# Kernel tuning notes

Hardware: AMD Instinct MI355X
Metric: run time of the kernel (lower is better)

Reference implementation:

```python
import jax, jax.numpy as jnp
import numpy as np

B, T, N_IN, N_REC, N_OUT = 64, 1000, 128, 1024, 64
PROP_E = 0.8
DT_OVER_TAU = 1.0 / 10.0  # dt=1, Tau=10


def dale_mask(n):
    e = int(PROP_E * n)
    m = np.tile(np.array([1.0] * e + [-1.0] * (n - e), dtype=np.float32), (n, 1))
    np.fill_diagonal(m, 0.0)
    return jnp.asarray(m)


def setup_inputs() -> dict:
    key = jax.random.key(0)
    ks = jax.random.split(key, 6)
    s = 1.0 / np.sqrt(N_REC)
    return {
        "x": jax.random.normal(ks[0], (B, T, N_IN), jnp.float32),
        "Wahx": jax.random.normal(ks[1], (N_REC, N_IN), jnp.float32) / np.sqrt(N_IN),
        "Wahh": jax.random.normal(ks[2], (N_REC, N_REC), jnp.float32) * s,
        "Wyh": jax.random.normal(ks[3], (N_OUT, N_REC), jnp.float32) * s,
        "bah": jax.random.normal(ks[4], (N_REC,), jnp.float32) * 0.01,
        "by": jax.random.normal(ks[5], (N_OUT,), jnp.float32) * 0.01,
        "ah0": jnp.zeros((N_REC,), jnp.float32),
        "mask": dale_mask(N_REC),
    }


def retanh(a):
    # 'retanh' activation: max(tanh(a), 0)
    return jnp.maximum(jnp.tanh(a), 0.0)


def reference(x, Wahx, Wahh, Wyh, bah, by, ah0, mask):
    # Dale-constrained effective recurrent weight: abs(W) * sign-mask
    Weff = jnp.abs(Wahh) * mask                       # [N, N]
    # precompute input drive for all timesteps: [B, T, N]
    xin = jnp.einsum('bti,ni->btn', x, Wahx) + bah
    ah_init = jnp.broadcast_to(ah0, (B, N_REC))

    def step(ah, xt):
        h = retanh(ah)
        ah_new = ah + DT_OVER_TAU * (-ah + h @ Weff.T + xt)
        return ah_new, retanh(ah_new)

    _, hs = jax.lax.scan(step, ah_init, jnp.swapaxes(xin, 0, 1))  # hs: [T, B, N]
    y = jnp.einsum('tbn,on->bto', hs, Wyh) + by       # [B, T, n_output]
    return y
```

## Files before the change

kernel.cpp:

```cpp
#include <hip/hip_runtime.h>
#include <hip/hip_bf16.h>
#include <stdint.h>


#define B_    64
#define T_    1000
#define NIN   128
#define NREC  1024
#define NOUT  64
#define GROUPS  4
#define MEMBERS 64
#define BPG   16
#define NSL   16

#define DT    0.1f

typedef short  bf16x8 __attribute__((ext_vector_type(8)));
typedef float  f32x4  __attribute__((ext_vector_type(4)));

#define SCOPE __HIP_MEMORY_SCOPE_AGENT

#define XB_OFF     0
#define XB_BYTES   (B_ * T_ * NIN * 2)
#define HBUF_OFF   (XB_OFF + XB_BYTES)
#define HBUF_BYTES (GROUPS * 2 * BPG * NREC * 2)

#define TAGMASK 0x8000000080000000ull

union U16B { unsigned long long q[2]; bf16x8 s; };

__device__ __forceinline__ unsigned short f2bf(float f) {
    unsigned u = __float_as_uint(f);
    unsigned r = u + 0x7fffu + ((u >> 16) & 1u);
    return (unsigned short)(r >> 16);
}
__device__ __forceinline__ unsigned pack2(float lo, float hi) {
    return (unsigned)f2bf(lo) | ((unsigned)f2bf(hi) << 16);
}

__global__ void cast_x_kernel(const float* __restrict__ x, unsigned short* __restrict__ xb, int n4) {
    int i = blockIdx.x * blockDim.x + threadIdx.x;
    int stride = gridDim.x * blockDim.x;
    for (; i < n4; i += stride) {
        float4 v = ((const float4*)x)[i];
        unsigned lo = pack2(v.x, v.y);
        unsigned hi = pack2(v.z, v.w);
        ((uint2*)xb)[i] = make_uint2(lo, hi);
    }
}

__global__ __launch_bounds__(256, 1)
void rnn_main(const float* __restrict__ Wahx, const float* __restrict__ Wahh,
              const float* __restrict__ Wyh,  const float* __restrict__ bah,
              const float* __restrict__ by,   const float* __restrict__ ah0,
              const float* __restrict__ mask,
              const unsigned short* __restrict__ xb,
              unsigned short* __restrict__ hbuf,
              float* __restrict__ y)
{
    __shared__ unsigned short weff[NSL * NREC];
    __shared__ unsigned short wahxs[NSL * NIN];
    __shared__ unsigned short wyhs[NREC];
    __shared__ float red[4][2][64][4];

    const int tid  = threadIdx.x;
    const int w    = tid >> 6;
    const int lane = tid & 63;
    const int bid  = blockIdx.x;
    const int g    = bid & 3;
    const int m    = bid >> 2;

    for (int cc = 0; cc < 8; ++cc) {
        int cid = cc * 256 + tid;
        int rl = cid >> 7;
        int k  = (cid & 127) * 8;
        const float* wr = Wahh + (m * NSL + rl) * NREC + k;
        const float* mr = mask + (m * NSL + rl) * NREC + k;
        float4 a0 = *(const float4*)wr;     float4 a1 = *(const float4*)(wr + 4);
        float4 m0 = *(const float4*)mr;     float4 m1 = *(const float4*)(mr + 4);
        uint4 pk;
        pk.x = pack2(fabsf(a0.x) * m0.x, fabsf(a0.y) * m0.y);
        pk.y = pack2(fabsf(a0.z) * m0.z, fabsf(a0.w) * m0.w);
        pk.z = pack2(fabsf(a1.x) * m1.x, fabsf(a1.y) * m1.y);
        pk.w = pack2(fabsf(a1.z) * m1.z, fabsf(a1.w) * m1.w);
        int byte = (rl * 2048 + k * 2) ^ ((rl & 7) << 4);
        *(uint4*)((char*)weff + byte) = pk;
    }
    {
        int rl = tid >> 4;
        int k  = (tid & 15) * 8;
        const float* wr = Wahx + (m * NSL + rl) * NIN + k;
        float4 a0 = *(const float4*)wr;  float4 a1 = *(const float4*)(wr + 4);
        uint4 pk;
        pk.x = pack2(a0.x, a0.y); pk.y = pack2(a0.z, a0.w);
        pk.z = pack2(a1.x, a1.y); pk.w = pack2(a1.z, a1.w);
        int byte = (rl * 256 + k * 2) ^ ((rl & 7) << 4);
        *(uint4*)((char*)wahxs + byte) = pk;
    }
    if (tid < 128) {
        int k = tid * 8;
        const float* wr = Wyh + m * NREC + k;
        float4 a0 = *(const float4*)wr;  float4 a1 = *(const float4*)(wr + 4);
        uint4 pk;
        pk.x = pack2(a0.x, a0.y); pk.y = pack2(a0.z, a0.w);
        pk.z = pack2(a1.x, a1.y); pk.w = pack2(a1.z, a1.w);
        *(uint4*)((char*)wyhs + k * 2) = pk;
    }

    const int b_loc = tid >> 4;
    const int nl    = tid & 15;
    const int n_g   = m * NSL + nl;
    float ahv  = ah0[n_g];
    float bahv = bah[n_g];
    float byv  = by[m];

    {
        float th = tanhf(ahv);
        float h0 = th > 0.f ? th : 0.f;
        unsigned hb = f2bf(h0);
        unsigned nb = __shfl_down(hb, 1);
        if ((nl & 1) == 0) {
            unsigned w32 = hb | (nb << 16);
            int eidx = ((g * 2 + 0) * BPG + b_loc) * NREC + n_g;
            __hip_atomic_store((unsigned*)hbuf + (eidx >> 1), w32, __ATOMIC_RELAXED, SCOPE);
        }
    }
    __syncthreads();

    const int bcol = lane & 15;
    const int khi  = (lane >> 4) * 8;

    for (int t = 0; t <= T_; ++t) {
        bf16x8 xf, axf;
        if (t < T_) {
            int i = w * 32 + khi;
            xf = *(const bf16x8*)(xb + ((size_t)(g * BPG + bcol) * T_ + t) * NIN + i);
            int byte = (bcol * 256 + i * 2) ^ ((bcol & 7) << 4);
            axf = *(const bf16x8*)((const char*)wahxs + byte);
        }

        const int slot = t & 1;
        const unsigned long long want = ((t >> 1) & 1) ? TAGMASK : 0ull;
        const unsigned long long* hq =
            (const unsigned long long*)(hbuf + ((g * 2 + slot) * BPG + bcol) * NREC);

        U16B u[8];
        unsigned pend = 0xFFu;
        for (;;) {
            #pragma unroll
            for (int c = 0; c < 8; ++c) {
                if (pend & (1u << c)) {
                    int k = w * 256 + c * 32 + khi;
                    u[c].q[0] = __hip_atomic_load(hq + (k >> 2),     __ATOMIC_RELAXED, SCOPE);
                    u[c].q[1] = __hip_atomic_load(hq + (k >> 2) + 1, __ATOMIC_RELAXED, SCOPE);
                }
            }
            unsigned np = 0u;
            #pragma unroll
            for (int c = 0; c < 8; ++c) {
                if (pend & (1u << c)) {
                    unsigned long long d = ((u[c].q[0] ^ want) | (u[c].q[1] ^ want)) & TAGMASK;
                    np |= d ? (1u << c) : 0u;
                }
            }
            pend = np;
            if (!__any(pend != 0u)) break;
            __builtin_amdgcn_s_sleep(1);
        }
        bf16x8 bfrag[8];
        #pragma unroll
        for (int c = 0; c < 8; ++c) {
            u[c].q[0] &= ~TAGMASK;
            u[c].q[1] &= ~TAGMASK;
            bfrag[c] = u[c].s;
        }

        f32x4 acc = {0.f, 0.f, 0.f, 0.f};
        if (t < T_) {
            f32x4 a0 = {0.f, 0.f, 0.f, 0.f};
            f32x4 a1 = {0.f, 0.f, 0.f, 0.f};
            a0 = __builtin_amdgcn_mfma_f32_16x16x32_bf16(axf, xf, a0, 0, 0, 0);
            #pragma unroll
            for (int c = 0; c < 4; ++c) {
                int k = w * 256 + c * 32 + khi;
                int byte = (bcol * 2048 + k * 2) ^ ((bcol & 7) << 4);
                bf16x8 af = *(const bf16x8*)((const char*)weff + byte);
                a0 = __builtin_amdgcn_mfma_f32_16x16x32_bf16(af, bfrag[c], a0, 0, 0, 0);
            }
            #pragma unroll
            for (int c = 4; c < 8; ++c) {
                int k = w * 256 + c * 32 + khi;
                int byte = (bcol * 2048 + k * 2) ^ ((bcol & 7) << 4);
                bf16x8 af = *(const bf16x8*)((const char*)weff + byte);
                a1 = __builtin_amdgcn_mfma_f32_16x16x32_bf16(af, bfrag[c], a1, 0, 0, 0);
            }
            acc = a0 + a1;
        }

        *(f32x4*)&red[w][0][lane][0] = acc;
        __syncthreads();

        if (t < T_) {
            int src = ((nl >> 2) << 4) | b_loc;
            int reg = nl & 3;
            float r = red[0][0][src][reg] + red[1][0][src][reg]
                    + red[2][0][src][reg] + red[3][0][src][reg];
            ahv = 0.9f * ahv + DT * (r + bahv);
            float th = tanhf(ahv);
            float h  = th > 0.f ? th : 0.f;
            unsigned hb = f2bf(h);
            unsigned nb = __shfl_down(hb, 1);
            if ((nl & 1) == 0) {
                unsigned tagw = (unsigned)(((t + 1) >> 1) & 1) << 31;
                unsigned w32 = hb | (nb << 16) | tagw;
                int eidx = ((g * 2 + (slot ^ 1)) * BPG + b_loc) * NREC + n_g;
                __hip_atomic_store((unsigned*)hbuf + (eidx >> 1), w32, __ATOMIC_RELAXED, SCOPE);
            }
        }

        if (t >= 1) {
            f32x4 accy = {0.f, 0.f, 0.f, 0.f};
            #pragma unroll
            for (int c = 0; c < 8; ++c) {
                int k = w * 256 + c * 32 + khi;
                bf16x8 af = *(const bf16x8*)((const char*)wyhs + k * 2);
                accy = __builtin_amdgcn_mfma_f32_16x16x32_bf16(af, bfrag[c], accy, 0, 0, 0);
            }
            *(f32x4*)&red[w][1][lane][0] = accy;
            __syncthreads();
            if (tid < BPG) {
                float yv = red[0][1][tid][0] + red[1][1][tid][0]
                         + red[2][1][tid][0] + red[3][1][tid][0] + byv;
                __builtin_nontemporal_store(yv, &y[((size_t)(g * BPG + tid) * T_ + (t - 1)) * NOUT + m]);
            }
        } else {
            __syncthreads();
        }
    }
}

extern "C" void kernel_launch(void* const* d_in, const int* in_sizes, int n_in,
                              void* d_out, int out_size, void* d_ws, size_t ws_size,
                              hipStream_t stream) {
    const float* x    = (const float*)d_in[0];
    const float* Wahx = (const float*)d_in[1];
    const float* Wahh = (const float*)d_in[2];
    const float* Wyh  = (const float*)d_in[3];
    const float* bah  = (const float*)d_in[4];
    const float* by   = (const float*)d_in[5];
    const float* ah0  = (const float*)d_in[6];
    const float* mask = (const float*)d_in[7];
    float* y = (float*)d_out;
    char* ws = (char*)d_ws;
    unsigned short* xb   = (unsigned short*)(ws + XB_OFF);
    unsigned short* hbuf = (unsigned short*)(ws + HBUF_OFF);

    (void)in_sizes; (void)n_in; (void)out_size; (void)ws_size;

    hipMemsetAsync(hbuf, 0xFF, HBUF_BYTES, stream);
    cast_x_kernel<<<dim3(2048), dim3(256), 0, stream>>>(x, xb, (B_ * T_ * NIN) / 4);
    rnn_main<<<dim3(GROUPS * MEMBERS), dim3(256), 0, stream>>>(
        Wahx, Wahh, Wyh, bah, by, ah0, mask, xb, hbuf, y);
}
```

Baseline: 3.175 ms.

## Halve workgroup count by assigning 32 recurrent neurons per workgroup

Each workgroup now owns 32 recurrent neurons and two output channels instead of 16 and one, so only 128 workgroups take part in the per-step cross-workgroup handoff through global memory instead of 256. Every wave issues twice the MFMAs per step on the same loaded h fragments, and each thread updates two neuron states. The aim is to cut synchronization and polling traffic and to reuse each h load across more work. The cost is a longer per-step critical path inside each workgroup and more LDS use for weights.

```diff
diff --git a/kernel.cpp b/kernel.cpp
--- a/kernel.cpp
+++ b/kernel.cpp
@@ -9,9 +9,9 @@
 #define NREC  1024
 #define NOUT  64
 #define GROUPS  4
-#define MEMBERS 64
+#define MEMBERS 32
 #define BPG   16
-#define NSL   16
+#define NSL   32
 
 #define DT    0.1f
 
@@ -60,8 +60,8 @@
 {
     __shared__ unsigned short weff[NSL * NREC];
     __shared__ unsigned short wahxs[NSL * NIN];
-    __shared__ unsigned short wyhs[NREC];
-    __shared__ float red[4][2][64][4];
+    __shared__ unsigned short wyhs[2 * NREC];
+    __shared__ float red[4][3][64][4];
 
     const int tid  = threadIdx.x;
     const int w    = tid >> 6;
@@ -70,7 +70,7 @@
     const int g    = bid & 3;
     const int m    = bid >> 2;
 
-    for (int cc = 0; cc < 8; ++cc) {
+    for (int cc = 0; cc < 16; ++cc) {
         int cid = cc * 256 + tid;
         int rl = cid >> 7;
         int k  = (cid & 127) * 8;
@@ -86,9 +86,10 @@
         int byte = (rl * 2048 + k * 2) ^ ((rl & 7) << 4);
         *(uint4*)((char*)weff + byte) = pk;
     }
-    {
-        int rl = tid >> 4;
-        int k  = (tid & 15) * 8;
+    for (int cc = 0; cc < 2; ++cc) {
+        int cid = cc * 256 + tid;
+        int rl = cid >> 4;
+        int k  = (cid & 15) * 8;
         const float* wr = Wahx + (m * NSL + rl) * NIN + k;
         float4 a0 = *(const float4*)wr;  float4 a1 = *(const float4*)(wr + 4);
         uint4 pk;
@@ -97,32 +98,35 @@
         int byte = (rl * 256 + k * 2) ^ ((rl & 7) << 4);
         *(uint4*)((char*)wahxs + byte) = pk;
     }
-    if (tid < 128) {
-        int k = tid * 8;
-        const float* wr = Wyh + m * NREC + k;
+    {
+        int row = tid >> 7;
+        int k   = (tid & 127) * 8;
+        const float* wr = Wyh + (2 * m + row) * NREC + k;
         float4 a0 = *(const float4*)wr;  float4 a1 = *(const float4*)(wr + 4);
         uint4 pk;
         pk.x = pack2(a0.x, a0.y); pk.y = pack2(a0.z, a0.w);
         pk.z = pack2(a1.x, a1.y); pk.w = pack2(a1.z, a1.w);
-        *(uint4*)((char*)wyhs + k * 2) = pk;
+        *(uint4*)((char*)wyhs + (row * 1024 + k) * 2) = pk;
     }
 
     const int b_loc = tid >> 4;
     const int nl    = tid & 15;
-    const int n_g   = m * NSL + nl;
-    float ahv  = ah0[n_g];
-    float bahv = bah[n_g];
-    float byv  = by[m];
+    const int n_g0  = m * NSL + nl;
+    const int n_g1  = n_g0 + 16;
+    float ahv0 = ah0[n_g0], ahv1 = ah0[n_g1];
+    float bahv0 = bah[n_g0], bahv1 = bah[n_g1];
+    float byv0 = by[2 * m], byv1 = by[2 * m + 1];
 
     {
-        float th = tanhf(ahv);
-        float h0 = th > 0.f ? th : 0.f;
-        unsigned hb = f2bf(h0);
-        unsigned nb = __shfl_down(hb, 1);
+        float t0 = tanhf(ahv0);  float h0 = t0 > 0.f ? t0 : 0.f;
+        float t1 = tanhf(ahv1);  float h1 = t1 > 0.f ? t1 : 0.f;
+        unsigned hb0 = f2bf(h0), hb1 = f2bf(h1);
+        unsigned nb0 = __shfl_down(hb0, 1), nb1 = __shfl_down(hb1, 1);
         if ((nl & 1) == 0) {
-            unsigned w32 = hb | (nb << 16);
-            int eidx = ((g * 2 + 0) * BPG + b_loc) * NREC + n_g;
-            __hip_atomic_store((unsigned*)hbuf + (eidx >> 1), w32, __ATOMIC_RELAXED, SCOPE);
+            int e0 = ((g * 2 + 0) * BPG + b_loc) * NREC + n_g0;
+            int e1 = ((g * 2 + 0) * BPG + b_loc) * NREC + n_g1;
+            __hip_atomic_store((unsigned*)hbuf + (e0 >> 1), hb0 | (nb0 << 16), __ATOMIC_RELAXED, SCOPE);
+            __hip_atomic_store((unsigned*)hbuf + (e1 >> 1), hb1 | (nb1 << 16), __ATOMIC_RELAXED, SCOPE);
         }
     }
     __syncthreads();
@@ -131,12 +135,14 @@
     const int khi  = (lane >> 4) * 8;
 
     for (int t = 0; t <= T_; ++t) {
-        bf16x8 xf, axf;
+        bf16x8 xf, axf0, axf1;
         if (t < T_) {
             int i = w * 32 + khi;
             xf = *(const bf16x8*)(xb + ((size_t)(g * BPG + bcol) * T_ + t) * NIN + i);
-            int byte = (bcol * 256 + i * 2) ^ ((bcol & 7) << 4);
-            axf = *(const bf16x8*)((const char*)wahxs + byte);
+            int by0 = (bcol * 256 + i * 2) ^ ((bcol & 7) << 4);
+            int by1 = ((bcol + 16) * 256 + i * 2) ^ ((bcol & 7) << 4);
+            axf0 = *(const bf16x8*)((const char*)wahxs + by0);
+            axf1 = *(const bf16x8*)((const char*)wahxs + by1);
         }
 
         const int slot = t & 1;
@@ -175,46 +181,62 @@
             bfrag[c] = u[c].s;
         }
 
-        f32x4 acc = {0.f, 0.f, 0.f, 0.f};
+        f32x4 acc0 = {0.f, 0.f, 0.f, 0.f};
+        f32x4 acc1 = {0.f, 0.f, 0.f, 0.f};
         if (t < T_) {
-            f32x4 a0 = {0.f, 0.f, 0.f, 0.f};
-            f32x4 a1 = {0.f, 0.f, 0.f, 0.f};
-            a0 = __builtin_amdgcn_mfma_f32_16x16x32_bf16(axf, xf, a0, 0, 0, 0);
+            f32x4 p00 = {0.f, 0.f, 0.f, 0.f}, p01 = {0.f, 0.f, 0.f, 0.f};
+            f32x4 p10 = {0.f, 0.f, 0.f, 0.f}, p11 = {0.f, 0.f, 0.f, 0.f};
+            p00 = __builtin_amdgcn_mfma_f32_16x16x32_bf16(axf0, xf, p00, 0, 0, 0);
+            p10 = __builtin_amdgcn_mfma_f32_16x16x32_bf16(axf1, xf, p10, 0, 0, 0);
             #pragma unroll
             for (int c = 0; c < 4; ++c) {
                 int k = w * 256 + c * 32 + khi;
-                int byte = (bcol * 2048 + k * 2) ^ ((bcol & 7) << 4);
-                bf16x8 af = *(const bf16x8*)((const char*)weff + byte);
-                a0 = __builtin_amdgcn_mfma_f32_16x16x32_bf16(af, bfrag[c], a0, 0, 0, 0);
+                int by0 = (bcol * 2048 + k * 2) ^ ((bcol & 7) << 4);
+                int by1 = ((bcol + 16) * 2048 + k * 2) ^ ((bcol & 7) << 4);
+                bf16x8 af0 = *(const bf16x8*)((const char*)weff + by0);
+                bf16x8 af1 = *(const bf16x8*)((const char*)weff + by1);
+                p00 = __builtin_amdgcn_mfma_f32_16x16x32_bf16(af0, bfrag[c], p00, 0, 0, 0);
+                p10 = __builtin_amdgcn_mfma_f32_16x16x32_bf16(af1, bfrag[c], p10, 0, 0, 0);
             }
             #pragma unroll
             for (int c = 4; c < 8; ++c) {
                 int k = w * 256 + c * 32 + khi;
-                int byte = (bcol * 2048 + k * 2) ^ ((bcol & 7) << 4);
-                bf16x8 af = *(const bf16x8*)((const char*)weff + byte);
-                a1 = __builtin_amdgcn_mfma_f32_16x16x32_bf16(af, bfrag[c], a1, 0, 0, 0);
-            }
-            acc = a0 + a1;
-        }
-
-        *(f32x4*)&red[w][0][lane][0] = acc;
+                int by0 = (bcol * 2048 + k * 2) ^ ((bcol & 7) << 4);
+                int by1 = ((bcol + 16) * 2048 + k * 2) ^ ((bcol & 7) << 4);
+                bf16x8 af0 = *(const bf16x8*)((const char*)weff + by0);
+                bf16x8 af1 = *(const bf16x8*)((const char*)weff + by1);
+                p01 = __builtin_amdgcn_mfma_f32_16x16x32_bf16(af0, bfrag[c], p01, 0, 0, 0);
+                p11 = __builtin_amdgcn_mfma_f32_16x16x32_bf16(af1, bfrag[c], p11, 0, 0, 0);
+            }
+            acc0 = p00 + p01;
+            acc1 = p10 + p11;
+        }
+
+        *(f32x4*)&red[w][0][lane][0] = acc0;
+        *(f32x4*)&red[w][1][lane][0] = acc1;
         __syncthreads();
 
         if (t < T_) {
             int src = ((nl >> 2) << 4) | b_loc;
             int reg = nl & 3;
-            float r = red[0][0][src][reg] + red[1][0][src][reg]
-                    + red[2][0][src][reg] + red[3][0][src][reg];
-            ahv = 0.9f * ahv + DT * (r + bahv);
-            float th = tanhf(ahv);
-            float h  = th > 0.f ? th : 0.f;
-            unsigned hb = f2bf(h);
-            unsigned nb = __shfl_down(hb, 1);
+            float r0 = red[0][0][src][reg] + red[1][0][src][reg]
+                     + red[2][0][src][reg] + red[3][0][src][reg];
+            float r1 = red[0][1][src][reg] + red[1][1][src][reg]
+                     + red[2][1][src][reg] + red[3][1][src][reg];
+            ahv0 = 0.9f * ahv0 + DT * (r0 + bahv0);
+            ahv1 = 0.9f * ahv1 + DT * (r1 + bahv1);
+            float t0 = tanhf(ahv0);  float h0 = t0 > 0.f ? t0 : 0.f;
+            float t1 = tanhf(ahv1);  float h1 = t1 > 0.f ? t1 : 0.f;
+            unsigned hb0 = f2bf(h0), hb1 = f2bf(h1);
+            unsigned nb0 = __shfl_down(hb0, 1), nb1 = __shfl_down(hb1, 1);
             if ((nl & 1) == 0) {
                 unsigned tagw = (unsigned)(((t + 1) >> 1) & 1) << 31;
-                unsigned w32 = hb | (nb << 16) | tagw;
-                int eidx = ((g * 2 + (slot ^ 1)) * BPG + b_loc) * NREC + n_g;
-                __hip_atomic_store((unsigned*)hbuf + (eidx >> 1), w32, __ATOMIC_RELAXED, SCOPE);
+                int e0 = ((g * 2 + (slot ^ 1)) * BPG + b_loc) * NREC + n_g0;
+                int e1 = ((g * 2 + (slot ^ 1)) * BPG + b_loc) * NREC + n_g1;
+                __hip_atomic_store((unsigned*)hbuf + (e0 >> 1),
+                                   hb0 | (nb0 << 16) | tagw, __ATOMIC_RELAXED, SCOPE);
+                __hip_atomic_store((unsigned*)hbuf + (e1 >> 1),
+                                   hb1 | (nb1 << 16) | tagw, __ATOMIC_RELAXED, SCOPE);
             }
         }
 
@@ -223,15 +245,22 @@
             #pragma unroll
             for (int c = 0; c < 8; ++c) {
                 int k = w * 256 + c * 32 + khi;
-                bf16x8 af = *(const bf16x8*)((const char*)wyhs + k * 2);
-                accy = __builtin_amdgcn_mfma_f32_16x16x32_bf16(af, bfrag[c], accy, 0, 0, 0);
-            }
-            *(f32x4*)&red[w][1][lane][0] = accy;
+                bf16x8 yaf = {0, 0, 0, 0, 0, 0, 0, 0};
+                if (bcol < 2)
+                    yaf = *(const bf16x8*)((const char*)wyhs + (bcol * 1024 + k) * 2);
+                accy = __builtin_amdgcn_mfma_f32_16x16x32_bf16(yaf, bfrag[c], accy, 0, 0, 0);
+            }
+            *(f32x4*)&red[w][2][lane][0] = accy;
             __syncthreads();
             if (tid < BPG) {
-                float yv = red[0][1][tid][0] + red[1][1][tid][0]
-                         + red[2][1][tid][0] + red[3][1][tid][0] + byv;
-                __builtin_nontemporal_store(yv, &y[((size_t)(g * BPG + tid) * T_ + (t - 1)) * NOUT + m]);
+                float yv0 = red[0][2][tid][0] + red[1][2][tid][0]
+                          + red[2][2][tid][0] + red[3][2][tid][0] + byv0;
+                float yv1 = red[0][2][tid][1] + red[1][2][tid][1]
+                          + red[2][2][tid][1] + red[3][2][tid][1] + byv1;
+                union { float f[2]; double d; } uu;
+                uu.f[0] = yv0; uu.f[1] = yv1;
+                __builtin_nontemporal_store(uu.d,
+                    (double*)&y[((size_t)(g * BPG + tid) * T_ + (t - 1)) * NOUT + 2 * m]);
             }
         } else {
             __syncthreads();
```

Result: slower. 3.543 ms (+11.6%).

## Give each wave a full batch slice and the full K, removing LDS reduction barriers

Applied to the files above, without the earlier changes.

The grid shrinks from 256 blocks (4 batch groups × 64 neuron slices) to 64 blocks. Each wave now owns 16 batch rows and accumulates over the full 1024-wide recurrent K in registers. This removes the cross-wave LDS reduction and both __syncthreads per timestep, and writes h as 64-bit tagged stores straight from the MFMA output layout. The cost is 4x more MFMA and polling-load work per wave, higher register pressure (32 bf16x8 fragments), and only a quarter as many CUs in use.

```diff
diff --git a/kernel.cpp b/kernel.cpp
--- a/kernel.cpp
+++ b/kernel.cpp
@@ -8,9 +8,7 @@
 #define NIN   128
 #define NREC  1024
 #define NOUT  64
-#define GROUPS  4
 #define MEMBERS 64
-#define BPG   16
 #define NSL   16
 
 #define DT    0.1f
@@ -23,7 +21,7 @@
 #define XB_OFF     0
 #define XB_BYTES   (B_ * T_ * NIN * 2)
 #define HBUF_OFF   (XB_OFF + XB_BYTES)
-#define HBUF_BYTES (GROUPS * 2 * BPG * NREC * 2)
+#define HBUF_BYTES (2 * B_ * NREC * 2)
 
 #define TAGMASK 0x8000000080000000ull
 
@@ -61,14 +59,11 @@
     __shared__ unsigned short weff[NSL * NREC];
     __shared__ unsigned short wahxs[NSL * NIN];
     __shared__ unsigned short wyhs[NREC];
-    __shared__ float red[4][2][64][4];
 
     const int tid  = threadIdx.x;
     const int w    = tid >> 6;
     const int lane = tid & 63;
-    const int bid  = blockIdx.x;
-    const int g    = bid & 3;
-    const int m    = bid >> 2;
+    const int m    = blockIdx.x;
 
     for (int cc = 0; cc < 8; ++cc) {
         int cid = cc * 256 + tid;
@@ -107,134 +102,118 @@
         *(uint4*)((char*)wyhs + k * 2) = pk;
     }
 
-    const int b_loc = tid >> 4;
-    const int nl    = tid & 15;
-    const int n_g   = m * NSL + nl;
-    float ahv  = ah0[n_g];
-    float bahv = bah[n_g];
-    float byv  = by[m];
-
-    {
-        float th = tanhf(ahv);
-        float h0 = th > 0.f ? th : 0.f;
-        unsigned hb = f2bf(h0);
-        unsigned nb = __shfl_down(hb, 1);
-        if ((nl & 1) == 0) {
-            unsigned w32 = hb | (nb << 16);
-            int eidx = ((g * 2 + 0) * BPG + b_loc) * NREC + n_g;
-            __hip_atomic_store((unsigned*)hbuf + (eidx >> 1), w32, __ATOMIC_RELAXED, SCOPE);
-        }
-    }
-    __syncthreads();
-
     const int bcol = lane & 15;
     const int khi  = (lane >> 4) * 8;
+    const int bg   = w * 16 + bcol;
+    const int nr0  = m * NSL + (lane >> 4) * 4;
+
+    f32x4 ahv, bahv;
+    #pragma unroll
+    for (int r = 0; r < 4; ++r) { ahv[r] = ah0[nr0 + r]; bahv[r] = bah[nr0 + r]; }
+    const float byv = by[m];
+
+    unsigned long long* const hq_base = (unsigned long long*)hbuf;
+
+    {
+        float h[4];
+        #pragma unroll
+        for (int r = 0; r < 4; ++r) { float th = tanhf(ahv[r]); h[r] = th > 0.f ? th : 0.f; }
+        unsigned lo = (unsigned)f2bf(h[0]) | ((unsigned)f2bf(h[1]) << 16);
+        unsigned hi = (unsigned)f2bf(h[2]) | ((unsigned)f2bf(h[3]) << 16);
+        unsigned long long wq = (unsigned long long)lo | ((unsigned long long)hi << 32);
+        __hip_atomic_store(hq_base + (((size_t)bg) << 8) + (nr0 >> 2), wq,
+                           __ATOMIC_RELAXED, SCOPE);
+    }
+    __syncthreads();
 
     for (int t = 0; t <= T_; ++t) {
-        bf16x8 xf, axf;
+        bf16x8 xf[4];
         if (t < T_) {
-            int i = w * 32 + khi;
-            xf = *(const bf16x8*)(xb + ((size_t)(g * BPG + bcol) * T_ + t) * NIN + i);
-            int byte = (bcol * 256 + i * 2) ^ ((bcol & 7) << 4);
-            axf = *(const bf16x8*)((const char*)wahxs + byte);
+            const unsigned short* xp = xb + ((size_t)bg * T_ + t) * NIN;
+            #pragma unroll
+            for (int cx = 0; cx < 4; ++cx)
+                xf[cx] = *(const bf16x8*)(xp + cx * 32 + khi);
         }
 
         const int slot = t & 1;
         const unsigned long long want = ((t >> 1) & 1) ? TAGMASK : 0ull;
-        const unsigned long long* hq =
-            (const unsigned long long*)(hbuf + ((g * 2 + slot) * BPG + bcol) * NREC);
-
-        U16B u[8];
-        unsigned pend = 0xFFu;
+        const unsigned long long* bq =
+            hq_base + (((size_t)(slot * B_ + bg)) << 8) + (khi >> 2);
+
+        U16B u[32];
+        unsigned pend = 0xFFFFFFFFu;
         for (;;) {
             #pragma unroll
-            for (int c = 0; c < 8; ++c) {
-                if (pend & (1u << c)) {
-                    int k = w * 256 + c * 32 + khi;
-                    u[c].q[0] = __hip_atomic_load(hq + (k >> 2),     __ATOMIC_RELAXED, SCOPE);
-                    u[c].q[1] = __hip_atomic_load(hq + (k >> 2) + 1, __ATOMIC_RELAXED, SCOPE);
-                }
+            for (int c = 0; c < 32; ++c) if (pend & (1u << c)) {
+                u[c].q[0] = __hip_atomic_load(bq + c * 8,     __ATOMIC_RELAXED, SCOPE);
+                u[c].q[1] = __hip_atomic_load(bq + c * 8 + 1, __ATOMIC_RELAXED, SCOPE);
             }
             unsigned np = 0u;
             #pragma unroll
-            for (int c = 0; c < 8; ++c) {
-                if (pend & (1u << c)) {
-                    unsigned long long d = ((u[c].q[0] ^ want) | (u[c].q[1] ^ want)) & TAGMASK;
-                    np |= d ? (1u << c) : 0u;
-                }
+            for (int c = 0; c < 32; ++c) if (pend & (1u << c)) {
+                if ((((u[c].q[0] ^ want) | (u[c].q[1] ^ want)) & TAGMASK) != 0ull)
+                    np |= (1u << c);
             }
             pend = np;
             if (!__any(pend != 0u)) break;
             __builtin_amdgcn_s_sleep(1);
         }
-        bf16x8 bfrag[8];
+        bf16x8 bfrag[32];
         #pragma unroll
-        for (int c = 0; c < 8; ++c) {
+        for (int c = 0; c < 32; ++c) {
             u[c].q[0] &= ~TAGMASK;
             u[c].q[1] &= ~TAGMASK;
             bfrag[c] = u[c].s;
         }
 
-        f32x4 acc = {0.f, 0.f, 0.f, 0.f};
         if (t < T_) {
-            f32x4 a0 = {0.f, 0.f, 0.f, 0.f};
-            f32x4 a1 = {0.f, 0.f, 0.f, 0.f};
-            a0 = __builtin_amdgcn_mfma_f32_16x16x32_bf16(axf, xf, a0, 0, 0, 0);
-            #pragma unroll
-            for (int c = 0; c < 4; ++c) {
-                int k = w * 256 + c * 32 + khi;
-                int byte = (bcol * 2048 + k * 2) ^ ((bcol & 7) << 4);
-                bf16x8 af = *(const bf16x8*)((const char*)weff + byte);
-                a0 = __builtin_amdgcn_mfma_f32_16x16x32_bf16(af, bfrag[c], a0, 0, 0, 0);
-            }
-            #pragma unroll
-            for (int c = 4; c < 8; ++c) {
-                int k = w * 256 + c * 32 + khi;
-                int byte = (bcol * 2048 + k * 2) ^ ((bcol & 7) << 4);
-                bf16x8 af = *(const bf16x8*)((const char*)weff + byte);
-                a1 = __builtin_amdgcn_mfma_f32_16x16x32_bf16(af, bfrag[c], a1, 0, 0, 0);
-            }
-            acc = a0 + a1;
-        }
-
-        *(f32x4*)&red[w][0][lane][0] = acc;
-        __syncthreads();
-
-        if (t < T_) {
-            int src = ((nl >> 2) << 4) | b_loc;
-            int reg = nl & 3;
-            float r = red[0][0][src][reg] + red[1][0][src][reg]
-                    + red[2][0][src][reg] + red[3][0][src][reg];
-            ahv = 0.9f * ahv + DT * (r + bahv);
-            float th = tanhf(ahv);
-            float h  = th > 0.f ? th : 0.f;
-            unsigned hb = f2bf(h);
-            unsigned nb = __shfl_down(hb, 1);
-            if ((nl & 1) == 0) {
-                unsigned tagw = (unsigned)(((t + 1) >> 1) & 1) << 31;
-                unsigned w32 = hb | (nb << 16) | tagw;
-                int eidx = ((g * 2 + (slot ^ 1)) * BPG + b_loc) * NREC + n_g;
-                __hip_atomic_store((unsigned*)hbuf + (eidx >> 1), w32, __ATOMIC_RELAXED, SCOPE);
-            }
+            f32x4 z = {0.f, 0.f, 0.f, 0.f};
+            f32x4 ch[4] = {z, z, z, z};
+            #pragma unroll
+            for (int cx = 0; cx < 4; ++cx) {
+                int i = cx * 32 + khi;
+                int byx = (bcol * 256 + i * 2) ^ ((bcol & 7) << 4);
+                bf16x8 axf = *(const bf16x8*)((const char*)wahxs + byx);
+                ch[cx] = __builtin_amdgcn_mfma_f32_16x16x32_bf16(axf, xf[cx], ch[cx], 0, 0, 0);
+            }
+            #pragma unroll
+            for (int c = 0; c < 32; ++c) {
+                int k = c * 32 + khi;
+                int byw = (bcol * 2048 + k * 2) ^ ((bcol & 7) << 4);
+                bf16x8 af = *(const bf16x8*)((const char*)weff + byw);
+                ch[c & 3] = __builtin_amdgcn_mfma_f32_16x16x32_bf16(af, bfrag[c], ch[c & 3], 0, 0, 0);
+            }
+            f32x4 acc = (ch[0] + ch[1]) + (ch[2] + ch[3]);
+
+            const unsigned tagw = ((unsigned)(((t + 1) >> 1) & 1)) << 31;
+            float h[4];
+            #pragma unroll
+            for (int r = 0; r < 4; ++r) {
+                ahv[r] = 0.9f * ahv[r] + DT * (acc[r] + bahv[r]);
+                float th = tanhf(ahv[r]);
+                h[r] = th > 0.f ? th : 0.f;
+            }
+            unsigned lo = (unsigned)f2bf(h[0]) | ((unsigned)f2bf(h[1]) << 16) | tagw;
+            unsigned hi = (unsigned)f2bf(h[2]) | ((unsigned)f2bf(h[3]) << 16) | tagw;
+            unsigned long long wq = (unsigned long long)lo | ((unsigned long long)hi << 32);
+            __hip_atomic_store(hq_base + (((size_t)((slot ^ 1) * B_ + bg)) << 8) + (nr0 >> 2),
+                               wq, __ATOMIC_RELAXED, SCOPE);
         }
 
         if (t >= 1) {
-            f32x4 accy = {0.f, 0.f, 0.f, 0.f};
-            #pragma unroll
-            for (int c = 0; c < 8; ++c) {
-                int k = w * 256 + c * 32 + khi;
-                bf16x8 af = *(const bf16x8*)((const char*)wyhs + k * 2);
-                accy = __builtin_amdgcn_mfma_f32_16x16x32_bf16(af, bfrag[c], accy, 0, 0, 0);
-            }
-            *(f32x4*)&red[w][1][lane][0] = accy;
-            __syncthreads();
-            if (tid < BPG) {
-                float yv = red[0][1][tid][0] + red[1][1][tid][0]
-                         + red[2][1][tid][0] + red[3][1][tid][0] + byv;
-                __builtin_nontemporal_store(yv, &y[((size_t)(g * BPG + tid) * T_ + (t - 1)) * NOUT + m]);
-            }
-        } else {
-            __syncthreads();
+            f32x4 z = {0.f, 0.f, 0.f, 0.f};
+            f32x4 ych[4] = {z, z, z, z};
+            #pragma unroll
+            for (int c = 0; c < 32; ++c) {
+                bf16x8 wyf = *(const bf16x8*)((const char*)wyhs + (c * 32 + khi) * 2);
+                ych[c & 3] = __builtin_amdgcn_mfma_f32_16x16x32_bf16(wyf, bfrag[c], ych[c & 3], 0, 0, 0);
+            }
+            f32x4 accy = (ych[0] + ych[1]) + (ych[2] + ych[3]);
+            if (lane < 16) {
+                float yv = accy[0] + byv;
+                __builtin_nontemporal_store(yv,
+                    &y[((size_t)(w * 16 + lane) * T_ + (t - 1)) * NOUT + m]);
+            }
         }
     }
 }
@@ -259,6 +238,6 @@
 
     hipMemsetAsync(hbuf, 0xFF, HBUF_BYTES, stream);
     cast_x_kernel<<<dim3(2048), dim3(256), 0, stream>>>(x, xb, (B_ * T_ * NIN) / 4);
-    rnn_main<<<dim3(GROUPS * MEMBERS), dim3(256), 0, stream>>>(
+    rnn_main<<<dim3(MEMBERS), dim3(256), 0, stream>>>(
         Wahx, Wahh, Wyh, bah, by, ah0, mask, xb, hbuf, y);
 }
```

Result: slower. 8.898 ms (+180.2%).

## Drop per-step barrier and prefetch next hidden state right after publishing

Applied to the files above, without the earlier changes.

Double-buffers the shared reduction arrays by slot so each timestep needs one block barrier instead of two. The output-projection reduction is deferred by one step and finished after the loop. Loads of the next step's hidden state are issued right after the local hidden values are stored, so the spin-wait usually only checks tags on data already in registers. The output accumulator is also split into two independent MFMA chains. The risk is that the early loads often see stale tags and have to be reissued, and the deferred reduction adds some bookkeeping.

```diff
diff --git a/kernel.cpp b/kernel.cpp
--- a/kernel.cpp
+++ b/kernel.cpp
@@ -61,7 +61,8 @@
     __shared__ unsigned short weff[NSL * NREC];
     __shared__ unsigned short wahxs[NSL * NIN];
     __shared__ unsigned short wyhs[NREC];
-    __shared__ float red[4][2][64][4];
+    __shared__ float red0[2][4][64][4];
+    __shared__ float red1[2][4][64][4];
 
     const int tid  = threadIdx.x;
     const int w    = tid >> 6;
@@ -130,7 +131,24 @@
     const int bcol = lane & 15;
     const int khi  = (lane >> 4) * 8;
 
+    U16B u[8];
+    {
+        const unsigned long long* hq0 =
+            (const unsigned long long*)(hbuf + ((g * 2 + 0) * BPG + bcol) * NREC);
+        #pragma unroll
+        for (int c = 0; c < 8; ++c) {
+            int k = w * 256 + c * 32 + khi;
+            u[c].q[0] = __hip_atomic_load(hq0 + (k >> 2),     __ATOMIC_RELAXED, SCOPE);
+            u[c].q[1] = __hip_atomic_load(hq0 + (k >> 2) + 1, __ATOMIC_RELAXED, SCOPE);
+        }
+    }
+
     for (int t = 0; t <= T_; ++t) {
+        const int slot = t & 1;
+        const unsigned long long want = ((t >> 1) & 1) ? TAGMASK : 0ull;
+        const unsigned long long* hq =
+            (const unsigned long long*)(hbuf + ((g * 2 + slot) * BPG + bcol) * NREC);
+
         bf16x8 xf, axf;
         if (t < T_) {
             int i = w * 32 + khi;
@@ -139,33 +157,23 @@
             axf = *(const bf16x8*)((const char*)wahxs + byte);
         }
 
-        const int slot = t & 1;
-        const unsigned long long want = ((t >> 1) & 1) ? TAGMASK : 0ull;
-        const unsigned long long* hq =
-            (const unsigned long long*)(hbuf + ((g * 2 + slot) * BPG + bcol) * NREC);
-
-        U16B u[8];
         unsigned pend = 0xFFu;
         for (;;) {
-            #pragma unroll
-            for (int c = 0; c < 8; ++c) {
-                if (pend & (1u << c)) {
-                    int k = w * 256 + c * 32 + khi;
-                    u[c].q[0] = __hip_atomic_load(hq + (k >> 2),     __ATOMIC_RELAXED, SCOPE);
-                    u[c].q[1] = __hip_atomic_load(hq + (k >> 2) + 1, __ATOMIC_RELAXED, SCOPE);
-                }
-            }
             unsigned np = 0u;
             #pragma unroll
-            for (int c = 0; c < 8; ++c) {
-                if (pend & (1u << c)) {
-                    unsigned long long d = ((u[c].q[0] ^ want) | (u[c].q[1] ^ want)) & TAGMASK;
-                    np |= d ? (1u << c) : 0u;
-                }
+            for (int c = 0; c < 8; ++c) if (pend & (1u << c)) {
+                if ((((u[c].q[0] ^ want) | (u[c].q[1] ^ want)) & TAGMASK) != 0ull)
+                    np |= (1u << c);
             }
             pend = np;
             if (!__any(pend != 0u)) break;
             __builtin_amdgcn_s_sleep(1);
+            #pragma unroll
+            for (int c = 0; c < 8; ++c) if (pend & (1u << c)) {
+                int k = w * 256 + c * 32 + khi;
+                u[c].q[0] = __hip_atomic_load(hq + (k >> 2),     __ATOMIC_RELAXED, SCOPE);
+                u[c].q[1] = __hip_atomic_load(hq + (k >> 2) + 1, __ATOMIC_RELAXED, SCOPE);
+            }
         }
         bf16x8 bfrag[8];
         #pragma unroll
@@ -197,14 +205,14 @@
             acc = a0 + a1;
         }
 
-        *(f32x4*)&red[w][0][lane][0] = acc;
+        *(f32x4*)&red0[slot][w][lane][0] = acc;
         __syncthreads();
 
         if (t < T_) {
             int src = ((nl >> 2) << 4) | b_loc;
             int reg = nl & 3;
-            float r = red[0][0][src][reg] + red[1][0][src][reg]
-                    + red[2][0][src][reg] + red[3][0][src][reg];
+            float r = red0[slot][0][src][reg] + red0[slot][1][src][reg]
+                    + red0[slot][2][src][reg] + red0[slot][3][src][reg];
             ahv = 0.9f * ahv + DT * (r + bahv);
             float th = tanhf(ahv);
             float h  = th > 0.f ? th : 0.f;
@@ -216,26 +224,47 @@
                 int eidx = ((g * 2 + (slot ^ 1)) * BPG + b_loc) * NREC + n_g;
                 __hip_atomic_store((unsigned*)hbuf + (eidx >> 1), w32, __ATOMIC_RELAXED, SCOPE);
             }
+            const unsigned long long* hqn =
+                (const unsigned long long*)(hbuf + ((g * 2 + (slot ^ 1)) * BPG + bcol) * NREC);
+            #pragma unroll
+            for (int c = 0; c < 8; ++c) {
+                int k = w * 256 + c * 32 + khi;
+                u[c].q[0] = __hip_atomic_load(hqn + (k >> 2),     __ATOMIC_RELAXED, SCOPE);
+                u[c].q[1] = __hip_atomic_load(hqn + (k >> 2) + 1, __ATOMIC_RELAXED, SCOPE);
+            }
         }
 
         if (t >= 1) {
-            f32x4 accy = {0.f, 0.f, 0.f, 0.f};
-            #pragma unroll
-            for (int c = 0; c < 8; ++c) {
+            f32x4 y0 = {0.f, 0.f, 0.f, 0.f};
+            f32x4 y1 = {0.f, 0.f, 0.f, 0.f};
+            #pragma unroll
+            for (int c = 0; c < 4; ++c) {
                 int k = w * 256 + c * 32 + khi;
                 bf16x8 af = *(const bf16x8*)((const char*)wyhs + k * 2);
-                accy = __builtin_amdgcn_mfma_f32_16x16x32_bf16(af, bfrag[c], accy, 0, 0, 0);
-            }
-            *(f32x4*)&red[w][1][lane][0] = accy;
-            __syncthreads();
-            if (tid < BPG) {
-                float yv = red[0][1][tid][0] + red[1][1][tid][0]
-                         + red[2][1][tid][0] + red[3][1][tid][0] + byv;
-                __builtin_nontemporal_store(yv, &y[((size_t)(g * BPG + tid) * T_ + (t - 1)) * NOUT + m]);
-            }
-        } else {
-            __syncthreads();
-        }
+                y0 = __builtin_amdgcn_mfma_f32_16x16x32_bf16(af, bfrag[c], y0, 0, 0, 0);
+            }
+            #pragma unroll
+            for (int c = 4; c < 8; ++c) {
+                int k = w * 256 + c * 32 + khi;
+                bf16x8 af = *(const bf16x8*)((const char*)wyhs + k * 2);
+                y1 = __builtin_amdgcn_mfma_f32_16x16x32_bf16(af, bfrag[c], y1, 0, 0, 0);
+            }
+            *(f32x4*)&red1[slot][w][lane][0] = y0 + y1;
+        }
+
+        if (t >= 2 && tid < BPG) {
+            float yv = red1[slot ^ 1][0][tid][0] + red1[slot ^ 1][1][tid][0]
+                     + red1[slot ^ 1][2][tid][0] + red1[slot ^ 1][3][tid][0] + byv;
+            __builtin_nontemporal_store(yv, &y[((size_t)(g * BPG + tid) * T_ + (t - 2)) * NOUT + m]);
+        }
+    }
+
+    __syncthreads();
+    if (tid < BPG) {
+        const int p = T_ & 1;
+        float yv = red1[p][0][tid][0] + red1[p][1][tid][0]
+                 + red1[p][2][tid][0] + red1[p][3][tid][0] + byv;
+        __builtin_nontemporal_store(yv, &y[((size_t)(g * BPG + tid) * T_ + (T_ - 1)) * NOUT + m]);
     }
 }
 
```

Measured after the change: 6.618 ms. +108.4%, slower.
